# Optimization experiments

Hardware: AMD Instinct MI355X
Metric: run time of the kernel (lower is better)

The kernel has to match this reference:

```python
import jax, jax.numpy as jnp
import numpy as np

B, S, D, H = 2, 2048, 1024, 16
DH = D // H


def setup_inputs() -> dict:
    key = jax.random.key(0)
    ks = jax.random.split(key, 6)
    scale = 1.0 / np.sqrt(D)
    x = jax.random.normal(ks[0], (B, S, D), dtype=jnp.float32)
    mask = jnp.tril(jnp.ones((S, S), dtype=jnp.int32))  # causal 0/1 mask
    Wq = jax.random.normal(ks[1], (D, D), dtype=jnp.float32) * scale
    Wk = jax.random.normal(ks[2], (D, D), dtype=jnp.float32) * scale
    Wv = jax.random.normal(ks[3], (D, D), dtype=jnp.float32) * scale
    Wo = jax.random.normal(ks[4], (D, D), dtype=jnp.float32) * scale
    z = jnp.zeros((D,), dtype=jnp.float32)
    return {"x": x, "mask": mask, "Wq": Wq, "bq": z, "Wk": Wk, "bk": z,
            "Wv": Wv, "bv": z, "Wo": Wo, "bo": z}


def reference(x, mask, Wq, bq, Wk, bk, Wv, bv, Wo, bo):
    # Linear projections (torch Linear: x @ W.T + b; here W stored as [in, out])
    Q = x @ Wq + bq
    K = x @ Wk + bk
    V = x @ Wv + bv
    # [B, S, D] -> [B, H, S, DH]
    Q = Q.reshape(B, S, H, DH).transpose(0, 2, 1, 3)
    K = K.reshape(B, S, H, DH).transpose(0, 2, 1, 3)
    V = V.reshape(B, S, H, DH).transpose(0, 2, 1, 3)
    # scores: [B, H, S, S]
    attn = jnp.einsum('bhqd,bhkd->bhqk', Q, K) / jnp.sqrt(jnp.float32(DH))
    attn = jnp.where(mask == 0, jnp.float32(-1e9), attn)
    scores = jax.nn.softmax(attn, axis=-1)
    # dropout is identity in eval mode
    out = jnp.einsum('bhqk,bhkd->bhqd', scores, V)
    out = out.transpose(0, 2, 1, 3).reshape(B, S, D)
    return out @ Wo + bo
```

## Files before the change

kernel.cpp:

```cpp
#include <hip/hip_runtime.h>
#include <hip/hip_bf16.h>


typedef short bf16x8 __attribute__((ext_vector_type(8)));
typedef float f32x4  __attribute__((ext_vector_type(4)));
typedef short s16x4  __attribute__((ext_vector_type(4)));

#define BB 2
#define SS 2048
#define DD 1024
#define HH 16
#define DHH 64

__device__ __forceinline__ unsigned short f2bf(float f) {
    unsigned u = __builtin_bit_cast(unsigned, f);
    u += 0x7FFFu + ((u >> 16) & 1u);
    return (unsigned short)(u >> 16);
}
__device__ __forceinline__ unsigned short f2bf_trunc(float f) {
    return (unsigned short)(__builtin_bit_cast(unsigned, f) >> 16);
}
__device__ __forceinline__ void cp16(const unsigned short* g, unsigned short* l) {
    __builtin_amdgcn_global_load_lds(
        (const __attribute__((address_space(1))) unsigned int*)(g),
        (__attribute__((address_space(3))) unsigned int*)(l), 16, 0, 0);
}

__global__ __launch_bounds__(256) void prep(
    const float* __restrict__ x,
    const float* __restrict__ w0, const float* __restrict__ w1,
    const float* __restrict__ w2, const float* __restrict__ w3,
    unsigned short* __restrict__ xbf, unsigned short* __restrict__ wt) {
    __shared__ float tile[64][65];
    const int bid = blockIdx.x;
    const int tid = threadIdx.x;
    if (bid < 4096) {
        int i = (bid * 256 + tid) * 4;
        float4 v = *reinterpret_cast<const float4*>(x + i);
        s16x4 p;
        p[0] = (short)f2bf(v.x); p[1] = (short)f2bf(v.y);
        p[2] = (short)f2bf(v.z); p[3] = (short)f2bf(v.w);
        *reinterpret_cast<s16x4*>(xbf + i) = p;
        return;
    }
    const int tb = bid - 4096;
    const int z  = tb >> 8;
    const int bx = (tb & 15) * 64, by = ((tb >> 4) & 15) * 64;
    const float* src = z == 0 ? w0 : z == 1 ? w1 : z == 2 ? w2 : w3;
    unsigned short* out = wt + (size_t)z * (DD * DD);
    const int tx = tid & 63, ty = tid >> 6;
    #pragma unroll
    for (int i = 0; i < 64; i += 4)
        tile[ty + i][tx] = src[(size_t)(by + ty + i) * DD + bx + tx];
    __syncthreads();
    #pragma unroll
    for (int i = 0; i < 64; i += 4)
        out[(size_t)(bx + ty + i) * DD + by + tx] = f2bf(tile[tx][ty + i]);
}

__global__ __launch_bounds__(256, 2) void gemm_qkv(
    const unsigned short* __restrict__ A, const unsigned short* __restrict__ Wt,
    const float* __restrict__ b0, const float* __restrict__ b1,
    const float* __restrict__ b2,
    unsigned short* __restrict__ d0, unsigned short* __restrict__ d1,
    unsigned short* __restrict__ d2) {
    __shared__ __align__(16) unsigned short As_[2][128 * 64];
    __shared__ __align__(16) unsigned short Bs_[2][192 * 64];

    const int tid  = threadIdx.x;
    const int lane = tid & 63;
    const int w    = tid >> 6;
    const int col  = lane & 15;
    const int quad = lane >> 4;
    const int wm   = (w >> 1) * 64;
    const int wn   = (w & 1) * 96;
    const int mb   = blockIdx.y * 128;
    const int nb   = blockIdx.x * 192;

    const int r8 = lane >> 3, gg = lane & 7;
    const int srcoff = ((gg ^ r8) * 8);
    const int cswz = col & 7;
    const int pos0 = (quad       ^ cswz) * 8;
    const int pos1 = ((4 + quad) ^ cswz) * 8;

    f32x4 acc[4][6];
    #pragma unroll
    for (int i = 0; i < 4; i++)
        #pragma unroll
        for (int j = 0; j < 6; j++) acc[i][j] = (f32x4){0.f, 0.f, 0.f, 0.f};

    auto stage = [&](int b, int kt) {
        #pragma unroll
        for (int i = 0; i < 4; i++) {
            int rb = w * 32 + i * 8;
            cp16(A + (size_t)(mb + rb + r8) * 1024 + kt + srcoff,
                 As_[b] + rb * 64);
        }
        #pragma unroll
        for (int i = 0; i < 6; i++) {
            int rb = w * 48 + i * 8;
            cp16(Wt + (size_t)(nb + rb + r8) * 1024 + kt + srcoff,
                 Bs_[b] + rb * 64);
        }
    };

    int cur = 0;
    stage(0, 0);
    __syncthreads();

    for (int kt = 0; kt < 1024; kt += 64) {
        if (kt + 64 < 1024) stage(cur ^ 1, kt + 64);
        const unsigned short* Ab = As_[cur];
        const unsigned short* Bb = Bs_[cur];
        bf16x8 bq0[6], bq1[6];
        #pragma unroll
        for (int j = 0; j < 6; j++) {
            const unsigned short* bp = Bb + (wn + j * 16 + col) * 64;
            bq0[j] = *reinterpret_cast<const bf16x8*>(bp + pos0);
            bq1[j] = *reinterpret_cast<const bf16x8*>(bp + pos1);
        }
        #pragma unroll
        for (int mi = 0; mi < 4; mi++) {
            const unsigned short* ap = Ab + (wm + mi * 16 + col) * 64;
            bf16x8 a0 = *reinterpret_cast<const bf16x8*>(ap + pos0);
            bf16x8 a1 = *reinterpret_cast<const bf16x8*>(ap + pos1);
            #pragma unroll
            for (int j = 0; j < 6; j++) {
                acc[mi][j] = __builtin_amdgcn_mfma_f32_16x16x32_bf16(a0, bq0[j], acc[mi][j], 0, 0, 0);
                acc[mi][j] = __builtin_amdgcn_mfma_f32_16x16x32_bf16(a1, bq1[j], acc[mi][j], 0, 0, 0);
            }
        }
        __syncthreads();
        cur ^= 1;
    }

    const float QSCALE = 0.125f * 1.44269504f;
    #pragma unroll
    for (int mi = 0; mi < 4; mi++) {
        int mg = mb + wm + mi * 16 + quad * 4;
        #pragma unroll
        for (int nj = 0; nj < 6; nj++) {
            int ng = nb + wn + nj * 16 + col;
            int sel = ng >> 10, n2 = ng & 1023;
            int h = n2 >> 6, dd2 = n2 & 63;
            int b = mg >> 11, s = mg & 2047;
            int bh = b * HH + h;
            const float* bp = sel == 0 ? b0 : sel == 1 ? b1 : b2;
            float bbv = bp[n2];
            if (sel == 0) {
                #pragma unroll
                for (int r = 0; r < 4; r++)
                    d0[((size_t)bh * SS + s + r) * DHH + dd2] = f2bf((acc[mi][nj][r] + bbv) * QSCALE);
            } else if (sel == 1) {
                #pragma unroll
                for (int r = 0; r < 4; r++)
                    d1[((size_t)bh * SS + s + r) * DHH + dd2] = f2bf(acc[mi][nj][r] + bbv);
            } else {
                s16x4 pack;
                #pragma unroll
                for (int r = 0; r < 4; r++) pack[r] = (short)f2bf(acc[mi][nj][r] + bbv);
                *reinterpret_cast<s16x4*>(d2 + ((size_t)bh * DHH + dd2) * SS + s) = pack;
            }
        }
    }
}

__global__ __launch_bounds__(256) void gemm_out(
    const unsigned short* __restrict__ A, const unsigned short* __restrict__ Wt,
    const float* __restrict__ b0, float* __restrict__ d0f) {
    __shared__ __align__(16) unsigned short As_[2][128 * 64];
    __shared__ __align__(16) unsigned short Bs_[2][128 * 64];

    const int tid  = threadIdx.x;
    const int lane = tid & 63;
    const int w    = tid >> 6;
    const int col  = lane & 15;
    const int quad = lane >> 4;
    const int wm   = (w >> 1) * 64;
    const int wn   = (w & 1) * 64;

    const int flat = blockIdx.y * 8 + blockIdx.x;
    const int swz  = (flat & 7) * 32 + (flat >> 3);
    const int mb   = (swz >> 3) * 128;
    const int nb   = (swz & 7) * 128;

    const int r8 = lane >> 3, gg = lane & 7;
    const int srcoff = ((gg ^ r8) * 8);
    const int cswz = col & 7;
    const int pos0 = (quad       ^ cswz) * 8;
    const int pos1 = ((4 + quad) ^ cswz) * 8;

    f32x4 acc[4][4];
    #pragma unroll
    for (int i = 0; i < 4; i++)
        #pragma unroll
        for (int j = 0; j < 4; j++) acc[i][j] = (f32x4){0.f, 0.f, 0.f, 0.f};

    auto stage = [&](int b, int kt) {
        #pragma unroll
        for (int it = 0; it < 4; it++) {
            int row = w * 32 + it * 8;
            cp16(A  + (size_t)(mb + row + r8) * 1024 + kt + srcoff, As_[b] + row * 64);
            cp16(Wt + (size_t)(nb + row + r8) * 1024 + kt + srcoff, Bs_[b] + row * 64);
        }
    };

    int cur = 0;
    stage(0, 0);
    __syncthreads();

    for (int kt = 0; kt < 1024; kt += 64) {
        if (kt + 64 < 1024) stage(cur ^ 1, kt + 64);
        const unsigned short* Ab = As_[cur];
        const unsigned short* Bb = Bs_[cur];
        bf16x8 bq0[4], bq1[4];
        #pragma unroll
        for (int j = 0; j < 4; j++) {
            const unsigned short* bp = Bb + (wn + j * 16 + col) * 64;
            bq0[j] = *reinterpret_cast<const bf16x8*>(bp + pos0);
            bq1[j] = *reinterpret_cast<const bf16x8*>(bp + pos1);
        }
        #pragma unroll
        for (int i = 0; i < 4; i++) {
            const unsigned short* ap = Ab + (wm + i * 16 + col) * 64;
            bf16x8 a0 = *reinterpret_cast<const bf16x8*>(ap + pos0);
            bf16x8 a1 = *reinterpret_cast<const bf16x8*>(ap + pos1);
            #pragma unroll
            for (int j = 0; j < 4; j++) {
                acc[i][j] = __builtin_amdgcn_mfma_f32_16x16x32_bf16(a0, bq0[j], acc[i][j], 0, 0, 0);
                acc[i][j] = __builtin_amdgcn_mfma_f32_16x16x32_bf16(a1, bq1[j], acc[i][j], 0, 0, 0);
            }
        }
        __syncthreads();
        cur ^= 1;
    }

    #pragma unroll
    for (int i = 0; i < 4; i++) {
        int mg = mb + wm + i * 16 + quad * 4;
        #pragma unroll
        for (int j = 0; j < 4; j++) {
            int ng = nb + wn + j * 16 + col;
            float bbv = b0[ng];
            #pragma unroll
            for (int r = 0; r < 4; r++)
                d0f[(size_t)(mg + r) * 1024 + ng] = acc[i][j][r] + bbv;
        }
    }
}

__global__ __launch_bounds__(256, 4) void attn(
    const unsigned short* __restrict__ Q, const unsigned short* __restrict__ K,
    const unsigned short* __restrict__ Vt, unsigned short* __restrict__ O) {
    __shared__ __align__(16) unsigned short Ks[2][64 * 64];
    __shared__ __align__(16) unsigned short Vs[2][64 * 64];

    const int tid  = threadIdx.x;
    const int lane = tid & 63;
    const int w    = tid >> 6;
    const int col  = lane & 15;
    const int quad = lane >> 4;
    const int bh   = blockIdx.x & 31;
    const int qt   = 31 - (blockIdx.x >> 5);
    const int qb   = qt * 64;
    const int r8 = lane >> 3, gg = lane & 7;
    const int srcoff = ((gg ^ r8) * 8);
    const int cswz = col & 7;
    const int pos0 = (quad       ^ cswz) * 8;
    const int pos1 = ((4 + quad) ^ cswz) * 8;

    bf16x8 onesf;
    #pragma unroll
    for (int j = 0; j < 8; j++) onesf[j] = (col == 0) ? (short)0x3F80 : (short)0;

    const int qrow = qb + w * 16 + col;
    const size_t qbase = ((size_t)bh * SS + qrow) * DHH;
    bf16x8 qlo = *reinterpret_cast<const bf16x8*>(Q + qbase + quad * 8);
    bf16x8 qhi = *reinterpret_cast<const bf16x8*>(Q + qbase + 32 + quad * 8);

    f32x4 o[5];
    #pragma unroll
    for (int d = 0; d < 5; d++) o[d] = (f32x4){0.f, 0.f, 0.f, 0.f};
    float m_i = 0.0f;

    const int ntiles = qt + 1;
    for (int t0 = 0; t0 < ntiles; t0 += 2) {
        const bool two = (t0 + 1 < ntiles);
        __syncthreads();
        #pragma unroll
        for (int it = 0; it < 2; it++) {
            int drow = w * 16 + it * 8;
            int skey = (w >> 1) * 32 + it * 16 + (r8 >> 2) * 8 + (w & 1) * 4 + (r8 & 3);
            cp16(K  + ((size_t)bh * SS + t0 * 64 + skey) * DHH + srcoff,
                 Ks[0] + drow * 64);
            cp16(Vt + ((size_t)bh * DHH + drow + r8) * SS + t0 * 64 + srcoff,
                 Vs[0] + drow * 64);
        }
        if (two) {
            #pragma unroll
            for (int it = 0; it < 2; it++) {
                int drow = w * 16 + it * 8;
                int skey = (w >> 1) * 32 + it * 16 + (r8 >> 2) * 8 + (w & 1) * 4 + (r8 & 3);
                cp16(K  + ((size_t)bh * SS + (t0 + 1) * 64 + skey) * DHH + srcoff,
                     Ks[1] + drow * 64);
                cp16(Vt + ((size_t)bh * DHH + drow + r8) * SS + (t0 + 1) * 64 + srcoff,
                     Vs[1] + drow * 64);
            }
        }
        __syncthreads();

        const float negm = -m_i;
        const f32x4 zinit = (f32x4){negm, negm, negm, negm};
        f32x4 sc[8];
        #pragma unroll
        for (int nt = 0; nt < 4; nt++) {
            int krow = nt * 16 + col;
            bf16x8 klo = *reinterpret_cast<const bf16x8*>(Ks[0] + krow * 64 + pos0);
            bf16x8 khi = *reinterpret_cast<const bf16x8*>(Ks[0] + krow * 64 + pos1);
            f32x4 z = zinit;
            z = __builtin_amdgcn_mfma_f32_16x16x32_bf16(klo, qlo, z, 0, 0, 0);
            z = __builtin_amdgcn_mfma_f32_16x16x32_bf16(khi, qhi, z, 0, 0, 0);
            sc[nt] = z;
        }
        if (two) {
            #pragma unroll
            for (int nt = 0; nt < 4; nt++) {
                int krow = nt * 16 + col;
                bf16x8 klo = *reinterpret_cast<const bf16x8*>(Ks[1] + krow * 64 + pos0);
                bf16x8 khi = *reinterpret_cast<const bf16x8*>(Ks[1] + krow * 64 + pos1);
                f32x4 z = zinit;
                z = __builtin_amdgcn_mfma_f32_16x16x32_bf16(klo, qlo, z, 0, 0, 0);
                z = __builtin_amdgcn_mfma_f32_16x16x32_bf16(khi, qhi, z, 0, 0, 0);
                sc[4 + nt] = z;
            }
        }
        if (t0 == qt || (two && t0 + 1 == qt)) {
            const int sb = (t0 == qt) ? 0 : 4;
            const int tb = (t0 == qt) ? t0 : t0 + 1;
            #pragma unroll
            for (int nt = 0; nt < 4; nt++) {
                #pragma unroll
                for (int r = 0; r < 4; r++) {
                    int kg = tb * 64 + (nt >> 1) * 32 + quad * 8 + (nt & 1) * 4 + r;
                    if (kg > qrow) sc[sb + nt][r] = -3.0e38f;
                }
            }
        }
        float mx = fmaxf(fmaxf(sc[0][0], sc[0][1]), fmaxf(sc[0][2], sc[0][3]));
        #pragma unroll
        for (int nt = 1; nt < 4; nt++)
            mx = fmaxf(mx, fmaxf(fmaxf(sc[nt][0], sc[nt][1]), fmaxf(sc[nt][2], sc[nt][3])));
        if (two) {
            #pragma unroll
            for (int nt = 4; nt < 8; nt++)
                mx = fmaxf(mx, fmaxf(fmaxf(sc[nt][0], sc[nt][1]), fmaxf(sc[nt][2], sc[nt][3])));
        }
        mx = fmaxf(mx, __shfl_xor(mx, 16));
        mx = fmaxf(mx, __shfl_xor(mx, 32));
        if (__any(mx > 8.0f)) {
            float dlt = (mx > 8.0f) ? mx : 0.0f;
            m_i += dlt;
            #pragma unroll
            for (int nt = 0; nt < 4; nt++)
                #pragma unroll
                for (int r = 0; r < 4; r++) sc[nt][r] -= dlt;
            if (two) {
                #pragma unroll
                for (int nt = 4; nt < 8; nt++)
                    #pragma unroll
                    for (int r = 0; r < 4; r++) sc[nt][r] -= dlt;
            }
            #pragma unroll
            for (int r = 0; r < 4; r++) {
                float a = exp2f(-__shfl(dlt, quad * 4 + r));
                #pragma unroll
                for (int d = 0; d < 5; d++) o[d][r] *= a;
            }
        }

        {
            bf16x8 pf0, pf1;
            #pragma unroll
            for (int j = 0; j < 8; j++) {
                pf0[j] = (short)f2bf_trunc(exp2f(sc[(j >> 2)][j & 3]));
                pf1[j] = (short)f2bf_trunc(exp2f(sc[2 + (j >> 2)][j & 3]));
            }
            #pragma unroll
            for (int dt = 0; dt < 4; dt++) {
                int rv = dt * 16 + col;
                bf16x8 vf0 = *reinterpret_cast<const bf16x8*>(Vs[0] + rv * 64 + pos0);
                bf16x8 vf1 = *reinterpret_cast<const bf16x8*>(Vs[0] + rv * 64 + pos1);
                o[dt] = __builtin_amdgcn_mfma_f32_16x16x32_bf16(pf0, vf0, o[dt], 0, 0, 0);
                o[dt] = __builtin_amdgcn_mfma_f32_16x16x32_bf16(pf1, vf1, o[dt], 0, 0, 0);
            }
            o[4] = __builtin_amdgcn_mfma_f32_16x16x32_bf16(pf0, onesf, o[4], 0, 0, 0);
            o[4] = __builtin_amdgcn_mfma_f32_16x16x32_bf16(pf1, onesf, o[4], 0, 0, 0);
        }
        if (two) {
            bf16x8 pf0, pf1;
            #pragma unroll
            for (int j = 0; j < 8; j++) {
                pf0[j] = (short)f2bf_trunc(exp2f(sc[4 + (j >> 2)][j & 3]));
                pf1[j] = (short)f2bf_trunc(exp2f(sc[6 + (j >> 2)][j & 3]));
            }
            #pragma unroll
            for (int dt = 0; dt < 4; dt++) {
                int rv = dt * 16 + col;
                bf16x8 vf0 = *reinterpret_cast<const bf16x8*>(Vs[1] + rv * 64 + pos0);
                bf16x8 vf1 = *reinterpret_cast<const bf16x8*>(Vs[1] + rv * 64 + pos1);
                o[dt] = __builtin_amdgcn_mfma_f32_16x16x32_bf16(pf0, vf0, o[dt], 0, 0, 0);
                o[dt] = __builtin_amdgcn_mfma_f32_16x16x32_bf16(pf1, vf1, o[dt], 0, 0, 0);
            }
            o[4] = __builtin_amdgcn_mfma_f32_16x16x32_bf16(pf0, onesf, o[4], 0, 0, 0);
            o[4] = __builtin_amdgcn_mfma_f32_16x16x32_bf16(pf1, onesf, o[4], 0, 0, 0);
        }
    }

    #pragma unroll
    for (int r = 0; r < 4; r++) {
        float lv = __shfl(o[4][r], lane & 48);
        float inv = 1.0f / lv;
        int sq = qb + w * 16 + quad * 4 + r;
        size_t base = ((size_t)(bh >> 4) * SS + sq) * DD + (size_t)(bh & 15) * DHH;
        #pragma unroll
        for (int dt = 0; dt < 4; dt++)
            O[base + dt * 16 + col] = f2bf(o[dt][r] * inv);
    }
}

extern "C" void kernel_launch(void* const* d_in, const int* in_sizes, int n_in,
                              void* d_out, int out_size, void* d_ws, size_t ws_size,
                              hipStream_t stream) {
    (void)in_sizes; (void)n_in; (void)out_size; (void)ws_size;
    const float* x  = (const float*)d_in[0];
    const float* Wq = (const float*)d_in[2];
    const float* bq = (const float*)d_in[3];
    const float* Wk = (const float*)d_in[4];
    const float* bk = (const float*)d_in[5];
    const float* Wv = (const float*)d_in[6];
    const float* bv = (const float*)d_in[7];
    const float* Wo = (const float*)d_in[8];
    const float* bo = (const float*)d_in[9];
    float* out = (float*)d_out;

    char* ws = (char*)d_ws;
    unsigned short* xbf = (unsigned short*)(ws);
    unsigned short* qws = (unsigned short*)(ws + ((size_t)8  << 20));
    unsigned short* kws = (unsigned short*)(ws + ((size_t)16 << 20));
    unsigned short* vws = (unsigned short*)(ws + ((size_t)24 << 20));
    unsigned short* wt  = (unsigned short*)(ws + ((size_t)32 << 20));
    unsigned short* ows = xbf;

    prep<<<dim3(5120), 256, 0, stream>>>(x, Wq, Wk, Wv, Wo, xbf, wt);
    gemm_qkv<<<dim3(16, 32), 256, 0, stream>>>(xbf, wt, bq, bk, bv,
                                               qws, kws, vws);
    attn<<<dim3(1024), 256, 0, stream>>>(qws, kws, vws, ows);
    gemm_out<<<dim3(8, 32), 256, 0, stream>>>(ows, wt + (size_t)3 * 1024 * 1024,
                                              bo, out);
}
```

Measured before the change: 185.9 us.

## Single-buffer K/V tiles with staggered per-tile prefetch and higher occupancy

The attention kernel stops processing two 64-key tiles per iteration with double-buffered LDS. It now handles one tile per iteration using single K and V buffers. The next K tile is issued right after QK^T finishes, and the next V tile after PV finishes, so each load overlaps the other half of the work. Halving LDS and registers lets launch bounds ask for 8 blocks per SM instead of 4, in exchange for more barriers per key tile and a shorter prefetch distance.

```diff
diff --git a/kernel.cpp b/kernel.cpp
--- a/kernel.cpp
+++ b/kernel.cpp
@@ -249,11 +249,11 @@
     }
 }
 
-__global__ __launch_bounds__(256, 4) void attn(
+__global__ __launch_bounds__(256, 8) void attn(
     const unsigned short* __restrict__ Q, const unsigned short* __restrict__ K,
     const unsigned short* __restrict__ Vt, unsigned short* __restrict__ O) {
-    __shared__ __align__(16) unsigned short Ks[2][64 * 64];
-    __shared__ __align__(16) unsigned short Vs[2][64 * 64];
+    __shared__ __align__(16) unsigned short Ks[64 * 64];
+    __shared__ __align__(16) unsigned short Vs[64 * 64];
 
     const int tid  = threadIdx.x;
     const int lane = tid & 63;
@@ -284,65 +284,53 @@
     float m_i = 0.0f;
 
     const int ntiles = qt + 1;
-    for (int t0 = 0; t0 < ntiles; t0 += 2) {
-        const bool two = (t0 + 1 < ntiles);
-        __syncthreads();
+
+    auto stageK = [&](int t) {
         #pragma unroll
         for (int it = 0; it < 2; it++) {
             int drow = w * 16 + it * 8;
             int skey = (w >> 1) * 32 + it * 16 + (r8 >> 2) * 8 + (w & 1) * 4 + (r8 & 3);
-            cp16(K  + ((size_t)bh * SS + t0 * 64 + skey) * DHH + srcoff,
-                 Ks[0] + drow * 64);
-            cp16(Vt + ((size_t)bh * DHH + drow + r8) * SS + t0 * 64 + srcoff,
-                 Vs[0] + drow * 64);
-        }
-        if (two) {
-            #pragma unroll
-            for (int it = 0; it < 2; it++) {
-                int drow = w * 16 + it * 8;
-                int skey = (w >> 1) * 32 + it * 16 + (r8 >> 2) * 8 + (w & 1) * 4 + (r8 & 3);
-                cp16(K  + ((size_t)bh * SS + (t0 + 1) * 64 + skey) * DHH + srcoff,
-                     Ks[1] + drow * 64);
-                cp16(Vt + ((size_t)bh * DHH + drow + r8) * SS + (t0 + 1) * 64 + srcoff,
-                     Vs[1] + drow * 64);
-            }
-        }
-        __syncthreads();
-
+            cp16(K + ((size_t)bh * SS + t * 64 + skey) * DHH + srcoff,
+                 Ks + drow * 64);
+        }
+    };
+    auto stageV = [&](int t) {
+        #pragma unroll
+        for (int it = 0; it < 2; it++) {
+            int drow = w * 16 + it * 8;
+            cp16(Vt + ((size_t)bh * DHH + drow + r8) * SS + t * 64 + srcoff,
+                 Vs + drow * 64);
+        }
+    };
+
+    stageK(0);
+    stageV(0);
+    __syncthreads();
+
+    for (int t = 0; t < ntiles; ++t) {
         const float negm = -m_i;
         const f32x4 zinit = (f32x4){negm, negm, negm, negm};
-        f32x4 sc[8];
+        f32x4 sc[4];
         #pragma unroll
         for (int nt = 0; nt < 4; nt++) {
             int krow = nt * 16 + col;
-            bf16x8 klo = *reinterpret_cast<const bf16x8*>(Ks[0] + krow * 64 + pos0);
-            bf16x8 khi = *reinterpret_cast<const bf16x8*>(Ks[0] + krow * 64 + pos1);
+            bf16x8 klo = *reinterpret_cast<const bf16x8*>(Ks + krow * 64 + pos0);
+            bf16x8 khi = *reinterpret_cast<const bf16x8*>(Ks + krow * 64 + pos1);
             f32x4 z = zinit;
             z = __builtin_amdgcn_mfma_f32_16x16x32_bf16(klo, qlo, z, 0, 0, 0);
             z = __builtin_amdgcn_mfma_f32_16x16x32_bf16(khi, qhi, z, 0, 0, 0);
             sc[nt] = z;
         }
-        if (two) {
+        __syncthreads();
+        if (t + 1 < ntiles) stageK(t + 1);
+
+        if (t == qt) {
             #pragma unroll
             for (int nt = 0; nt < 4; nt++) {
-                int krow = nt * 16 + col;
-                bf16x8 klo = *reinterpret_cast<const bf16x8*>(Ks[1] + krow * 64 + pos0);
-                bf16x8 khi = *reinterpret_cast<const bf16x8*>(Ks[1] + krow * 64 + pos1);
-                f32x4 z = zinit;
-                z = __builtin_amdgcn_mfma_f32_16x16x32_bf16(klo, qlo, z, 0, 0, 0);
-                z = __builtin_amdgcn_mfma_f32_16x16x32_bf16(khi, qhi, z, 0, 0, 0);
-                sc[4 + nt] = z;
-            }
-        }
-        if (t0 == qt || (two && t0 + 1 == qt)) {
-            const int sb = (t0 == qt) ? 0 : 4;
-            const int tb = (t0 == qt) ? t0 : t0 + 1;
-            #pragma unroll
-            for (int nt = 0; nt < 4; nt++) {
                 #pragma unroll
                 for (int r = 0; r < 4; r++) {
-                    int kg = tb * 64 + (nt >> 1) * 32 + quad * 8 + (nt & 1) * 4 + r;
-                    if (kg > qrow) sc[sb + nt][r] = -3.0e38f;
+                    int kg = t * 64 + (nt >> 1) * 32 + quad * 8 + (nt & 1) * 4 + r;
+                    if (kg > qrow) sc[nt][r] = -3.0e38f;
                 }
             }
         }
@@ -350,11 +338,6 @@
         #pragma unroll
         for (int nt = 1; nt < 4; nt++)
             mx = fmaxf(mx, fmaxf(fmaxf(sc[nt][0], sc[nt][1]), fmaxf(sc[nt][2], sc[nt][3])));
-        if (two) {
-            #pragma unroll
-            for (int nt = 4; nt < 8; nt++)
-                mx = fmaxf(mx, fmaxf(fmaxf(sc[nt][0], sc[nt][1]), fmaxf(sc[nt][2], sc[nt][3])));
-        }
         mx = fmaxf(mx, __shfl_xor(mx, 16));
         mx = fmaxf(mx, __shfl_xor(mx, 32));
         if (__any(mx > 8.0f)) {
@@ -364,12 +347,6 @@
             for (int nt = 0; nt < 4; nt++)
                 #pragma unroll
                 for (int r = 0; r < 4; r++) sc[nt][r] -= dlt;
-            if (two) {
-                #pragma unroll
-                for (int nt = 4; nt < 8; nt++)
-                    #pragma unroll
-                    for (int r = 0; r < 4; r++) sc[nt][r] -= dlt;
-            }
             #pragma unroll
             for (int r = 0; r < 4; r++) {
                 float a = exp2f(-__shfl(dlt, quad * 4 + r));
@@ -388,32 +365,16 @@
             #pragma unroll
             for (int dt = 0; dt < 4; dt++) {
                 int rv = dt * 16 + col;
-                bf16x8 vf0 = *reinterpret_cast<const bf16x8*>(Vs[0] + rv * 64 + pos0);
-                bf16x8 vf1 = *reinterpret_cast<const bf16x8*>(Vs[0] + rv * 64 + pos1);
+                bf16x8 vf0 = *reinterpret_cast<const bf16x8*>(Vs + rv * 64 + pos0);
+                bf16x8 vf1 = *reinterpret_cast<const bf16x8*>(Vs + rv * 64 + pos1);
                 o[dt] = __builtin_amdgcn_mfma_f32_16x16x32_bf16(pf0, vf0, o[dt], 0, 0, 0);
                 o[dt] = __builtin_amdgcn_mfma_f32_16x16x32_bf16(pf1, vf1, o[dt], 0, 0, 0);
             }
             o[4] = __builtin_amdgcn_mfma_f32_16x16x32_bf16(pf0, onesf, o[4], 0, 0, 0);
             o[4] = __builtin_amdgcn_mfma_f32_16x16x32_bf16(pf1, onesf, o[4], 0, 0, 0);
         }
-        if (two) {
-            bf16x8 pf0, pf1;
-            #pragma unroll
-            for (int j = 0; j < 8; j++) {
-                pf0[j] = (short)f2bf_trunc(exp2f(sc[4 + (j >> 2)][j & 3]));
-                pf1[j] = (short)f2bf_trunc(exp2f(sc[6 + (j >> 2)][j & 3]));
-            }
-            #pragma unroll
-            for (int dt = 0; dt < 4; dt++) {
-                int rv = dt * 16 + col;
-                bf16x8 vf0 = *reinterpret_cast<const bf16x8*>(Vs[1] + rv * 64 + pos0);
-                bf16x8 vf1 = *reinterpret_cast<const bf16x8*>(Vs[1] + rv * 64 + pos1);
-                o[dt] = __builtin_amdgcn_mfma_f32_16x16x32_bf16(pf0, vf0, o[dt], 0, 0, 0);
-                o[dt] = __builtin_amdgcn_mfma_f32_16x16x32_bf16(pf1, vf1, o[dt], 0, 0, 0);
-            }
-            o[4] = __builtin_amdgcn_mfma_f32_16x16x32_bf16(pf0, onesf, o[4], 0, 0, 0);
-            o[4] = __builtin_amdgcn_mfma_f32_16x16x32_bf16(pf1, onesf, o[4], 0, 0, 0);
-        }
+        __syncthreads();
+        if (t + 1 < ntiles) stageV(t + 1);
     }
 
     #pragma unroll
```

New measurement: 285.6 us. +53.6%, slower.
